# Performance work log

Measured on AMD Instinct MI355X. Metric: run time of the kernel, lower is better.

## Reference

```python
import jax, jax.numpy as jnp
import numpy as np

B, WS, DIM, HEADS, AGENT, PS = 128, 14, 256, 8, 49, 7
N = WS * WS


def conv(x, w, b, pad, groups=1):
    y = jax.lax.conv_general_dilated(x, w, (1, 1), [(pad, pad), (pad, pad)],
                                     dimension_numbers=('NCHW', 'OIHW', 'NCHW'),
                                     feature_group_count=groups)
    return y + b[None, :, None, None]


def bilinear_resize(x, oh, ow):
    # F.interpolate(mode='bilinear', align_corners=False) on last two dims
    ih, iw = x.shape[-2], x.shape[-1]
    def grid(ni, no):
        pos = np.maximum((np.arange(no) + 0.5) * (ni / no) - 0.5, 0.0)
        i0 = np.minimum(np.floor(pos).astype(np.int32), ni - 1)
        i1 = np.minimum(i0 + 1, ni - 1)
        return i0, i1, (pos - i0).astype(np.float32)
    i0h, i1h, lh = grid(ih, oh)
    i0w, i1w, lw = grid(iw, ow)
    xh = x[..., i0h, :] * (1.0 - lh)[:, None] + x[..., i1h, :] * lh[:, None]
    return xh[..., i0w] * (1.0 - lw) + xh[..., i1w] * lw


def rel_pos_index(h, w):
    coords = np.stack(np.meshgrid(np.arange(h), np.arange(w), indexing='ij')).reshape(2, -1)
    rel = (coords[:, :, None] - coords[:, None, :]).transpose(1, 2, 0).copy()
    rel[..., 0] += h - 1
    rel[..., 1] += w - 1
    rel[..., 0] *= 2 * w - 1
    return rel.sum(-1)  # (h*w, h*w)


def cbam(x, caa1_w, caa1_b, caa2_w, caa2_b, cam1_w, cam1_b, cam2_w, cam2_b, sa_w, sa_b):
    # ChannelAttention: both conv stacks act on 1x1 pooled maps -> only kernel centers matter
    avgp = x.mean((2, 3))
    t1 = jax.nn.relu(jnp.einsum('oi,bi->bo', caa1_w[:, :, 1, 1], avgp) + caa1_b)
    y1 = jax.nn.sigmoid(jnp.einsum('oi,bi->bo', caa2_w[:, :, 1, 1], t1) + caa2_b)
    mxp = x.max((2, 3))
    t2 = jax.nn.relu(jnp.einsum('oi,bi->bo', cam1_w[:, :, 0, 0], mxp) + cam1_b)
    y2 = jax.nn.sigmoid(jnp.einsum('oi,bi->bo', cam2_w[:, :, 0, 0], t2) + cam2_b)
    x = jax.nn.sigmoid(y1 + y2)[:, :, None, None] * x
    # Spatial attention
    mask = jnp.concatenate([x.mean(1, keepdims=True), x.max(1, keepdims=True)], axis=1)
    mask = jax.nn.sigmoid(conv(mask, sa_w, sa_b, 4))
    return x * mask


def chan_inter(x, ci1_w, ci1_b, bn_g, bn_b, ci2_w, ci2_b):
    # AdaptiveAvgPool2d(1) then 5x5 convs on 1x1 maps -> kernel-center matmuls; BN in eval mode
    p = x.mean((2, 3))
    t = jnp.einsum('oi,bi->bo', ci1_w[:, :, 2, 2], p) + ci1_b
    t = jax.nn.relu(bn_g * t * (1.0 / np.sqrt(1.0 + 1e-5)) + bn_b)
    return jnp.einsum('oi,bi->bo', ci2_w[:, :, 2, 2], t) + ci2_b


def setup_inputs() -> dict:
    key = jax.random.key(0)
    ks = jax.random.split(key, 40)
    d, r = DIM, DIM // 16
    p = lambda i, shape, s=0.02: jax.random.normal(ks[i], shape, jnp.float32) * s
    return {
        'x': jax.random.normal(ks[0], (B, N, d), jnp.float32),
        'h': WS,
        'w': WS,
        'lka_w': p(1, (3 * d, 1, 5, 5)), 'lka_b': p(2, (3 * d,)),
        'conv5_w': p(3, (d, d, 5, 5)), 'conv5_b': p(4, (d,)),
        'caa1_w': p(5, (r, d, 3, 3)), 'caa1_b': p(6, (r,)),
        'caa2_w': p(7, (d, r, 3, 3)), 'caa2_b': p(8, (d,)),
        'cam1_w': p(9, (r, d, 1, 1)), 'cam1_b': p(10, (r,)),
        'cam2_w': p(11, (d, r, 1, 1)), 'cam2_b': p(12, (d,)),
        'sa_w': p(13, (1, 2, 9, 9)), 'sa_b': p(14, (1,)),
        'ci1_w': p(15, (r, d, 5, 5)), 'ci1_b': p(16, (r,)),
        'bn_g': jnp.ones((r,), jnp.float32), 'bn_b': jnp.zeros((r,), jnp.float32),
        'ci2_w': p(17, (d, r, 5, 5)), 'ci2_b': p(18, (d,)),
        'rpb_table': p(19, ((2 * WS - 1) * (2 * WS - 1), HEADS)),
        'an_bias': p(20, (HEADS, AGENT, 7, 7)), 'na_bias': p(21, (HEADS, AGENT, 7, 7)),
        'ah_bias': p(22, (1, HEADS, AGENT, WS, 1)), 'aw_bias': p(23, (1, HEADS, AGENT, 1, WS)),
        'ha_bias': p(24, (1, HEADS, WS, 1, AGENT)), 'wa_bias': p(25, (1, HEADS, 1, WS, AGENT)),
        'dwc_w': p(26, (d, 1, 5, 5)), 'dwc_b': p(27, (d,)),
        'proj_w': p(28, (d, d)), 'proj_b': p(29, (d,)),
    }


def reference(x, h, w, lka_w, lka_b, conv5_w, conv5_b, caa1_w, caa1_b, caa2_w, caa2_b,
              cam1_w, cam1_b, cam2_w, cam2_b, sa_w, sa_b, ci1_w, ci1_b, bn_g, bn_b,
              ci2_w, ci2_b, rpb_table, an_bias, na_bias, ah_bias, aw_bias, ha_bias,
              wa_bias, dwc_w, dwc_b, proj_w, proj_b):
    b, n, c = x.shape
    heads, agent, ps = HEADS, AGENT, PS
    hd = c // heads
    scale = hd ** (-0.5)

    xc = jnp.transpose(x.reshape(b, h, w, c), (0, 3, 1, 2))  # (b,c,h,w)
    y = conv(xc, lka_w, lka_b, 2, groups=c)                   # depthwise, 3 outputs/group
    k_raw, v_raw, q_raw = y[:, :c], y[:, c:2 * c], y[:, 2 * c:]

    # v branch: conv5 then raw reshape-scramble (faithful to torch .reshape of NCHW), then CBAM
    v5 = jnp.transpose(conv(v_raw, conv5_w, conv5_b, 2).reshape(b, h, w, c), (0, 3, 1, 2))
    vc = cbam(v5, caa1_w, caa1_b, caa2_w, caa2_b, cam1_w, cam1_b, cam2_w, cam2_b, sa_w, sa_b)
    v_feat = jnp.transpose(vc.reshape(b, c, n), (0, 2, 1))    # (b,n,c)

    # adaptive avg/max pool 14->7 == exact 2x2 pooling
    at = q_raw.reshape(b, c, ps, h // ps, ps, w // ps).mean((3, 5)).reshape(b, c, agent).transpose(0, 2, 1)
    atk = k_raw.reshape(b, c, ps, h // ps, ps, w // ps).max((3, 5)).reshape(b, c, agent).transpose(0, 2, 1)

    # raw row-major reshapes of (b,c,h,w) into (b,n,heads,hd): faithful to torch
    q = q_raw.reshape(b, n, heads, hd).transpose(0, 2, 1, 3) * scale
    k = k_raw.reshape(b, n, heads, hd).transpose(0, 2, 1, 3)
    v = v_raw.reshape(b, n, heads, hd).transpose(0, 2, 1, 3)
    v1 = v_feat.reshape(b, n, heads, hd).transpose(0, 2, 1, 3)

    # full window attention with relative position bias
    idx = rel_pos_index(h, w)
    rpb = rpb_table[idx.reshape(-1)].reshape(n, n, heads).transpose(2, 0, 1)
    attn = jax.nn.softmax(jnp.einsum('bhid,bhjd->bhij', q, k) + rpb[None])
    x1 = jnp.einsum('bhij,bhjd->bhid', attn, v).transpose(0, 2, 1, 3).reshape(b, n, c)

    ar = x1.transpose(0, 2, 1).reshape(b, c, h, w)
    cmap = chan_inter(ar, ci1_w, ci1_b, bn_g, bn_b, ci2_w, ci2_b)  # (b,c)
    conv_x2 = jax.nn.sigmoid(cmap)[:, :, None, None] * jnp.transpose(q.reshape(b, h, w, c), (0, 3, 1, 2))

    # agent attention
    at_h = at.reshape(b, agent, heads, hd).transpose(0, 2, 1, 3)
    atk_h = atk.reshape(b, agent, heads, hd).transpose(0, 2, 1, 3)
    pb = bilinear_resize(an_bias, h, w).reshape(1, heads, agent, n) \
         + (ah_bias + aw_bias).reshape(1, heads, agent, n)
    agent_attn = jax.nn.softmax(jnp.einsum('bhad,bhnd->bhan', at_h * scale, k) + pb)
    agent_attn1 = jax.nn.softmax(jnp.einsum('bhad,bhnd->bhan', atk_h * scale, q) + pb)
    agent_v = jnp.einsum('bhan,bhnd->bhad', agent_attn, v1) + jnp.einsum('bhan,bhnd->bhad', agent_attn1, v)

    ab = bilinear_resize(na_bias, h, w).reshape(1, heads, agent, n).transpose(0, 1, 3, 2) \
         + (ha_bias + wa_bias).reshape(1, heads, n, agent)
    q_attn = jax.nn.softmax(jnp.einsum('bhnd,bhad->bhna', q * scale, at_h) + ab)
    k_attn = jax.nn.softmax(jnp.einsum('bhnd,bhad->bhna', k * scale, atk_h) + ab)
    xo = jnp.einsum('bhna,bhad->bhnd', q_attn + k_attn, agent_v).transpose(0, 2, 1, 3).reshape(b, n, c)

    xo = xo + jnp.transpose(conv(conv_x2, dwc_w, dwc_b, 2, groups=c), (0, 2, 3, 1)).reshape(b, n, c)
    qc = jnp.transpose(q.transpose(0, 2, 1, 3).reshape(b, h, w, c), (0, 3, 1, 2))
    xo = xo + jnp.transpose(conv(qc, dwc_w, dwc_b, 2, groups=c), (0, 2, 3, 1)).reshape(b, n, c)

    return xo @ proj_w.T + proj_b
```

## Files before the change

kernel.cpp:

```cpp
#include <hip/hip_runtime.h>

#define NB    128
#define NC    256
#define NPOS  196
#define NHEAD 8
#define NAG   49
#define YSTR  150528
#define VOFF  50176
#define QOFF  100352
#define SCL   0.17677669529663687f

#define WS_Y    0u
#define WS_V5   19267584u
#define WS_AT   25690112u
#define WS_ATK  27295744u
#define WS_CHG  28901376u
#define WS_CMAP 28934144u
#define WS_PBT  28966912u
#define WS_AB   29043744u
#define WS_X1S  29120576u
#define WS_AGV  29153344u
#define WS_XO   30758976u
#define WS_WT   37181504u
#define WS_CWT  37247040u

typedef __attribute__((ext_vector_type(8))) _Float16 half8;
typedef __attribute__((ext_vector_type(8))) short short8;
typedef __attribute__((ext_vector_type(4))) short short4v;
typedef __attribute__((ext_vector_type(4))) float f32x4;
typedef unsigned short ushort_t;
typedef unsigned int uint_t;

__device__ __forceinline__ float sigmoidf_(float x){ return 1.0f/(1.0f+__expf(-x)); }

__device__ __forceinline__ ushort_t f2h(float x){
  _Float16 h = (_Float16)x; return __builtin_bit_cast(ushort_t, h);
}
__device__ __forceinline__ float h2f(ushort_t u){
  return (float)__builtin_bit_cast(_Float16, u);
}

__device__ __forceinline__ float bilin7(const float* __restrict__ src, int i, int j){
  float pi = fmaxf(0.5f*(float)i - 0.25f, 0.f);
  int i0 = (int)pi; if (i0 > 6) i0 = 6;
  int i1 = i0 + 1;  if (i1 > 6) i1 = 6;
  float li = pi - (float)i0;
  float pj = fmaxf(0.5f*(float)j - 0.25f, 0.f);
  int j0 = (int)pj; if (j0 > 6) j0 = 6;
  int j1 = j0 + 1;  if (j1 > 6) j1 = 6;
  float lj = pj - (float)j0;
  float v00 = src[i0*7+j0], v01 = src[i0*7+j1];
  float v10 = src[i1*7+j0], v11 = src[i1*7+j1];
  float t0 = v00*(1.f-lj) + v01*lj;
  float t1 = v10*(1.f-lj) + v11*lj;
  return t0*(1.f-li) + t1*li;
}

__device__ __forceinline__ void conv5x5_row(const float* __restrict__ plane, int r,
                                            const float* __restrict__ w25, float* acc14){
  #pragma unroll
  for (int di = 0; di < 5; ++di){
    const float4* pr = (const float4*)(plane + (r+di)*20);
    float4 p0 = pr[0], p1 = pr[1], p2 = pr[2], p3 = pr[3], p4 = pr[4];
    float row[20] = {p0.x,p0.y,p0.z,p0.w, p1.x,p1.y,p1.z,p1.w, p2.x,p2.y,p2.z,p2.w,
                     p3.x,p3.y,p3.z,p3.w, p4.x,p4.y,p4.z,p4.w};
    #pragma unroll
    for (int dj = 0; dj < 5; ++dj){
      float w = w25[di*5+dj];
      #pragma unroll
      for (int j = 0; j < 14; ++j) acc14[j] = fmaf(row[j+dj], w, acc14[j]);
    }
  }
}

__global__ void k_pb(const float* __restrict__ an, const float* __restrict__ ah,
                     const float* __restrict__ aw, float* __restrict__ PBT){
  int t = blockIdx.x*256 + threadIdx.x;
  if (t >= NHEAD*NPOS*NAG) return;
  int a = t % NAG;
  int r = t / NAG;
  int n = r % NPOS;
  int h = r / NPOS;
  int i = n/14, j = n - (n/14)*14;
  float v = bilin7(an + ((size_t)h*NAG + a)*49, i, j);
  v += ah[((size_t)h*NAG + a)*14 + i] + aw[((size_t)h*NAG + a)*14 + j];
  PBT[t] = v;
}

__global__ void k_ab(const float* __restrict__ na, const float* __restrict__ ha,
                     const float* __restrict__ wa, float* __restrict__ AB){
  int t = blockIdx.x*256 + threadIdx.x;
  if (t >= NHEAD*NPOS*NAG) return;
  int a = t % NAG;
  int r = t / NAG;
  int n = r % NPOS;
  int h = r / NPOS;
  int i = n/14, j = n - (n/14)*14;
  float v = bilin7(na + ((size_t)h*NAG + a)*49, i, j);
  v += ha[((size_t)h*14 + i)*NAG + a] + wa[((size_t)h*14 + j)*NAG + a];
  AB[t] = v;
}

__global__ void k_wt(const float* __restrict__ pw, float* __restrict__ WT){
  int t = blockIdx.x*256 + threadIdx.x;
  if (t >= 65536) return;
  int k = t >> 8, c = t & 255;
  WT[t] = pw[c*256 + k];
}

__global__ void k_cw2(const float* __restrict__ cw, ushort_t* __restrict__ Wh){
  int t = blockIdx.x*256 + threadIdx.x;
  if (t >= 1638400) return;
  int ci = t & 255;
  int r  = t >> 8;
  int co = r & 255;
  int tap = r >> 8;
  Wh[t] = f2h(cw[((size_t)co*256 + ci)*25 + tap]);
}

__global__ __launch_bounds__(256) void k_lka(const float* __restrict__ x, const float* __restrict__ lw,
                                             const float* __restrict__ lb, float* __restrict__ Y){
  int b = blockIdx.x >> 3, gb = blockIdx.x & 7;
  int g0 = gb*32;
  __shared__ __align__(16) float pl[32*360];
  int tid = threadIdx.x;
  for (int t = tid; t < 32*360; t += 256) pl[t] = 0.f;
  __syncthreads();
  for (int t = tid; t < 32*196; t += 256){
    int gl = t & 31, s = t >> 5;
    int i = s/14, j = s - i*14;
    pl[gl*360 + (i+2)*20 + j + 2] = x[((size_t)b*196 + s)*256 + g0 + gl];
  }
  __syncthreads();
  for (int t = tid; t < 96*14; t += 256){
    int ocl = t/14, r = t - ocl*14;
    int o  = g0*3 + ocl;
    int gl = ocl/3;
    float w25[25];
    #pragma unroll
    for (int u = 0; u < 25; ++u) w25[u] = lw[o*25 + u];
    float acc[14];
    float bv = lb[o];
    #pragma unroll
    for (int j = 0; j < 14; ++j) acc[j] = bv;
    conv5x5_row(&pl[gl*360], r, w25, acc);
    float* dst = Y + ((size_t)b*768 + o)*196 + r*14;
    #pragma unroll
    for (int j = 0; j < 14; ++j) dst[j] = acc[j];
  }
}

__global__ __launch_bounds__(256, 2) void k_conv5(const float* __restrict__ Y,
    const ushort_t* __restrict__ Wh, const float* __restrict__ cb, float* __restrict__ V5){
  int b = blockIdx.x >> 2, cog = blockIdx.x & 3;
  int co0 = cog*64;
  __shared__ __align__(16) ushort_t Pt[360*40];
  __shared__ __align__(16) ushort_t Wsm[5*64*40];
  __shared__ float T[32*200];
  int tid  = threadIdx.x;
  int lane = tid & 63, wv = tid >> 6;
  int mrow = lane & 15, quad = lane >> 4;

  for (int t = tid; t < 7200; t += 256) ((uint_t*)Pt)[t] = 0;

  int prow[4];
  #pragma unroll
  for (int mt = 0; mt < 4; ++mt){
    int s = wv*64 + mt*16 + mrow;
    int p0 = 0;
    if (s < 196){ int i = s/14, j = s - i*14; p0 = i*20 + j; }
    prow[mt] = p0;
  }

  f32x4 acc[4][4];
  #pragma unroll
  for (int mt = 0; mt < 4; ++mt)
    #pragma unroll
    for (int nt = 0; nt < 4; ++nt) acc[mt][nt] = (f32x4){0.f,0.f,0.f,0.f};

  const float* src = Y + (size_t)b*YSTR + VOFF;
  int wco = tid >> 2, wpart = tid & 3;

  #pragma unroll 1
  for (int cc = 0; cc < 8; ++cc){
    __syncthreads();
    if (tid < 196){
      int s = tid; int i = s/14, j = s - i*14;
      int p = (i+2)*20 + (j+2);
      const float* s0 = src + (cc*32)*196 + s;
      #pragma unroll
      for (int cp = 0; cp < 16; ++cp){
        float v0 = s0[(2*cp)*196];
        float v1 = s0[(2*cp+1)*196];
        uint_t pk = (uint_t)f2h(v0) | ((uint_t)f2h(v1) << 16);
        int q = cp >> 2;
        *(uint_t*)&Pt[p*40 + (((q ^ p) & 3) << 3) + ((2*cp) & 7)] = pk;
      }
    }
    #pragma unroll 1
    for (int di = 0; di < 5; ++di){
      __syncthreads();
      #pragma unroll
      for (int tp = 0; tp < 5; ++tp){
        int tap = di*5 + tp;
        const short8 g = *(const short8*)(Wh + ((size_t)tap*256 + co0 + wco)*256 + cc*32 + wpart*8);
        *(short8*)&Wsm[(tp*64 + wco)*40 + (((wpart ^ wco) & 3) << 3)] = g;
      }
      __syncthreads();
      #pragma unroll
      for (int dj = 0; dj < 5; ++dj){
        half8 a[4], bb[4];
        #pragma unroll
        for (int nt = 0; nt < 4; ++nt){
          int co = nt*16 + mrow;
          bb[nt] = *(const half8*)&Wsm[(dj*64 + co)*40 + (((quad ^ co) & 3) << 3)];
        }
        #pragma unroll
        for (int mt = 0; mt < 4; ++mt){
          int p = prow[mt] + di*20 + dj;
          a[mt] = *(const half8*)&Pt[p*40 + (((quad ^ p) & 3) << 3)];
        }
        #pragma unroll
        for (int mt = 0; mt < 4; ++mt)
          #pragma unroll
          for (int nt = 0; nt < 4; ++nt)
            acc[mt][nt] = __builtin_amdgcn_mfma_f32_16x16x32_f16(a[mt], bb[nt], acc[mt][nt], 0, 0, 0);
      }
    }
  }

  #pragma unroll
  for (int hf = 0; hf < 2; ++hf){
    __syncthreads();
    #pragma unroll
    for (int ntl = 0; ntl < 2; ++ntl){
      int nt = hf*2 + ntl;
      int col = ntl*16 + mrow;
      #pragma unroll
      for (int mt = 0; mt < 4; ++mt){
        int sbase = wv*64 + mt*16 + quad*4;
        #pragma unroll
        for (int r = 0; r < 4; ++r){
          int s = sbase + r;
          if (s < 196) T[col*200 + s] = acc[mt][nt][r];
        }
      }
    }
    __syncthreads();
    for (int t = tid; t < 6272; t += 256){
      int cl = t / 196;
      int f = (co0 + hf*32)*196 + t;
      float val = T[t + cl*4] + cb[co0 + hf*32 + cl];
      V5[(size_t)b*50176 + (size_t)(f & 255)*196 + (f >> 8)] = val;
    }
  }
}

__global__ __launch_bounds__(256) void k_pool(const float* __restrict__ Y, float* __restrict__ AT, float* __restrict__ ATK){
  int b = blockIdx.x; int c = threadIdx.x;
  const float* qp = Y + ((size_t)b*768 + 512 + c)*196;
  const float* kp = Y + ((size_t)b*768 + c)*196;
  for (int a = 0; a < 49; ++a){
    int p1 = a/7, p2 = a - p1*7;
    int s = p1*28 + p2*2;
    float q0 = qp[s], q1 = qp[s+1], q2 = qp[s+14], q3 = qp[s+15];
    AT[((size_t)b*49 + a)*256 + c] = 0.25f*(q0+q1+q2+q3);
    float k0 = kp[s], k1 = kp[s+1], k2 = kp[s+14], k3 = kp[s+15];
    ATK[((size_t)b*49 + a)*256 + c] = fmaxf(fmaxf(k0,k1), fmaxf(k2,k3));
  }
}

__global__ __launch_bounds__(256) void k_cbam_a(const float* __restrict__ V5,
    const float* __restrict__ caa1w, const float* __restrict__ caa1b,
    const float* __restrict__ caa2w, const float* __restrict__ caa2b,
    const float* __restrict__ cam1w, const float* __restrict__ cam1b,
    const float* __restrict__ cam2w, const float* __restrict__ cam2b,
    float* __restrict__ CHG){
  int b = blockIdx.x, c = threadIdx.x;
  __shared__ float avg[256], mx[256], t1[16], t2[16];
  const float* pp = V5 + ((size_t)b*256 + c)*196;
  float s = 0.f, m = -1e30f;
  for (int i = 0; i < 196; ++i){ float v = pp[i]; s += v; m = fmaxf(m, v); }
  avg[c] = s * (1.0f/196.0f); mx[c] = m;
  __syncthreads();
  if (c < 16){
    float a1 = caa1b[c], a2 = cam1b[c];
    #pragma unroll 4
    for (int k = 0; k < 256; ++k){
      a1 = fmaf(caa1w[(c*256 + k)*9 + 4], avg[k], a1);
      a2 = fmaf(cam1w[c*256 + k], mx[k], a2);
    }
    t1[c] = fmaxf(a1, 0.f);
    t2[c] = fmaxf(a2, 0.f);
  }
  __syncthreads();
  float y1 = caa2b[c], y2 = cam2b[c];
  #pragma unroll
  for (int k = 0; k < 16; ++k){
    y1 = fmaf(caa2w[(c*16 + k)*9 + 4], t1[k], y1);
    y2 = fmaf(cam2w[c*16 + k], t2[k], y2);
  }
  CHG[b*256 + c] = sigmoidf_(sigmoidf_(y1) + sigmoidf_(y2));
}

__global__ __launch_bounds__(256) void k_cbam_b(float* __restrict__ V5, const float* __restrict__ CHG,
    const float* __restrict__ saw, const float* __restrict__ sab){
  int b = blockIdx.x; int tid = threadIdx.x;
  __shared__ float chg[256];
  __shared__ float mp[22*22], xp[22*22];
  __shared__ float mk[196];
  chg[tid] = CHG[b*256 + tid];
  for (int t = tid; t < 484; t += 256){ mp[t] = 0.f; xp[t] = 0.f; }
  __syncthreads();
  if (tid < 196){
    int i = tid/14, j = tid - i*14;
    float s = 0.f, m = -1e30f;
    const float* vb = V5 + (size_t)b*256*196 + tid;
    for (int c = 0; c < 256; ++c){
      float v = chg[c] * vb[c*196];
      s += v; m = fmaxf(m, v);
    }
    mp[(i+4)*22 + j+4] = s*(1.f/256.f);
    xp[(i+4)*22 + j+4] = m;
  }
  __syncthreads();
  if (tid < 196){
    int i = tid/14, j = tid - i*14;
    float acc = sab[0];
    for (int di = 0; di < 9; ++di){
      #pragma unroll
      for (int dj = 0; dj < 9; ++dj){
        acc = fmaf(mp[(i+di)*22 + j+dj], saw[di*9+dj], acc);
        acc = fmaf(xp[(i+di)*22 + j+dj], saw[81 + di*9+dj], acc);
      }
    }
    mk[tid] = sigmoidf_(acc);
  }
  __syncthreads();
  if (tid < 196){
    float m = mk[tid];
    float* vb = V5 + (size_t)b*256*196 + tid;
    for (int c = 0; c < 256; ++c) vb[c*196] = chg[c]*vb[c*196]*m;
  }
}

__global__ __launch_bounds__(256) void k_attn(const float* __restrict__ Y, const float* __restrict__ rpbt,
                                              float* __restrict__ X1S){
  int b = blockIdx.x >> 3, h = blockIdx.x & 7;
  __shared__ float rp[729];
  __shared__ float xs[196*33];
  int tid = threadIdx.x;
  for (int t = tid; t < 729; t += 256) rp[t] = rpbt[t*8 + h];
  __syncthreads();
  const float* yb = Y + (size_t)b*YSTR;
  if (tid < 196){
    int n = tid;
    float q[32];
    {
      const float4* q4 = (const float4*)(yb + QOFF + (size_t)n*256 + h*32);
      #pragma unroll
      for (int u = 0; u < 8; ++u){
        float4 v = q4[u];
        q[4*u] = v.x*SCL; q[4*u+1] = v.y*SCL; q[4*u+2] = v.z*SCL; q[4*u+3] = v.w*SCL;
      }
    }
    int ri = n/14, ci = n - ri*14;
    int bidx = (ri + 13)*27 + (ci + 13);
    float acc[32];
    #pragma unroll
    for (int d = 0; d < 32; ++d) acc[d] = 0.f;
    float l = 0.f;
    int rj = 0, cj = 0;
    for (int j = 0; j < 196; ++j){
      const float4* k4 = (const float4*)(yb + (size_t)j*256 + h*32);
      float s0 = 0.f, s1 = 0.f;
      #pragma unroll
      for (int u = 0; u < 8; u += 2){
        float4 a = k4[u], bb = k4[u+1];
        s0 = fmaf(q[4*u+0],a.x, fmaf(q[4*u+1],a.y, fmaf(q[4*u+2],a.z, fmaf(q[4*u+3],a.w, s0))));
        s1 = fmaf(q[4*u+4],bb.x, fmaf(q[4*u+5],bb.y, fmaf(q[4*u+6],bb.z, fmaf(q[4*u+7],bb.w, s1))));
      }
      float s = s0 + s1 + rp[bidx - rj*27 - cj];
      float p = __expf(s);
      l += p;
      const float4* v4 = (const float4*)(yb + VOFF + (size_t)j*256 + h*32);
      #pragma unroll
      for (int u = 0; u < 8; ++u){
        float4 vv = v4[u];
        acc[4*u]   = fmaf(p, vv.x, acc[4*u]);
        acc[4*u+1] = fmaf(p, vv.y, acc[4*u+1]);
        acc[4*u+2] = fmaf(p, vv.z, acc[4*u+2]);
        acc[4*u+3] = fmaf(p, vv.w, acc[4*u+3]);
      }
      if (++cj == 14){ cj = 0; ++rj; }
    }
    float inv = 1.f/l;
    #pragma unroll
    for (int d = 0; d < 32; ++d) xs[n*33 + d] = acc[d]*inv;
  }
  __syncthreads();
  if (tid < 32){
    float s = 0.f;
    for (int n = 0; n < 196; ++n) s += xs[n*33 + tid];
    X1S[(size_t)b*256 + h*32 + tid] = s*(1.f/196.f);
  }
}

__global__ __launch_bounds__(256) void k_cinter(const float* __restrict__ X1S,
    const float* __restrict__ ci1w, const float* __restrict__ ci1b,
    const float* __restrict__ bng, const float* __restrict__ bnb,
    const float* __restrict__ ci2w, const float* __restrict__ ci2b, float* __restrict__ CMAP){
  int b = blockIdx.x, c = threadIdx.x;
  __shared__ float p[256], tt[16];
  p[c] = X1S[b*256 + c];
  __syncthreads();
  if (c < 16){
    float a = ci1b[c];
    #pragma unroll 4
    for (int k = 0; k < 256; ++k) a = fmaf(ci1w[(c*256+k)*25 + 12], p[k], a);
    const float invs = 0.9999950000375f;
    tt[c] = fmaxf(fmaf(bng[c]*invs, a, bnb[c]), 0.f);
  }
  __syncthreads();
  float a = ci2b[c];
  #pragma unroll
  for (int k = 0; k < 16; ++k) a = fmaf(ci2w[(c*16+k)*25 + 12], tt[k], a);
  CMAP[b*256 + c] = sigmoidf_(a);
}

__global__ __launch_bounds__(256) void k_agentv(const float* __restrict__ Y, const float* __restrict__ V5,
    const float* __restrict__ AT, const float* __restrict__ ATK,
    const float* __restrict__ PBT, float* __restrict__ AGV){
  int b = blockIdx.x >> 3, h = blockIdx.x & 7;
  __shared__ __align__(16) ushort_t ST[64*232];
  __shared__ __align__(16) ushort_t R[8704];
  __shared__ float psum[4*64];
  __shared__ float inv0s[64], inv1s[64];
  int tid = threadIdx.x, wv = tid >> 6, lane = tid & 63;
  int mrow = lane & 15, quad = lane >> 4;
  const float* yb = Y + (size_t)b*YSTR;
  ushort_t* Kh = R;
  ushort_t* Ah = R + 6656;
  ushort_t* Vt = R;
  f32x4 out0[2], out1[2];

  for (int t = tid; t < 512; t += 256){
    int a = t >> 3, c2 = 208 + ((t & 7) << 1);
    *(uint_t*)&ST[a*232 + c2] = 0;
  }

  #pragma unroll 1
  for (int pass = 0; pass < 2; ++pass){
    for (int t = tid; t < 192; t += 256) ((uint_t*)Kh)[3136 + t] = 0;
    for (int t = tid; t < 240; t += 256) ((uint_t*)Ah)[784 + t] = 0;
    {
      const float* rsrc = yb + (pass ? QOFF : 0) + h*32;
      for (int t = tid; t < 3136; t += 256){
        int n = t >> 4, dp = (t & 15) << 1;
        const float2 v = *(const float2*)(rsrc + (size_t)n*256 + dp);
        ((uint_t*)Kh)[n*16 + (dp >> 1)] = (uint_t)f2h(v.x) | ((uint_t)f2h(v.y) << 16);
      }
      const float* asrc = (pass ? ATK : AT) + (size_t)b*49*256 + h*32;
      for (int t = tid; t < 784; t += 256){
        int a = t >> 4, dp = (t & 15) << 1;
        const float2 v = *(const float2*)(asrc + (size_t)a*256 + dp);
        ((uint_t*)Ah)[a*16 + (dp >> 1)] = (uint_t)f2h(v.x) | ((uint_t)f2h(v.y) << 16);
      }
    }
    __syncthreads();
    {
      float lscl = pass ? 0.03125f : SCL;
      int ag = wv*16 + mrow;
      half8 bfr = *(const half8*)&Ah[ag*32 + quad*8];
      #pragma unroll 1
      for (int mt = 0; mt < 13; ++mt){
        half8 afr = *(const half8*)&Kh[(mt*16 + mrow)*32 + quad*8];
        f32x4 c = (f32x4){0.f,0.f,0.f,0.f};
        c = __builtin_amdgcn_mfma_f32_16x16x32_f16(afr, bfr, c, 0, 0, 0);
        int n0 = mt*16 + quad*4;
        short4v pk;
        #pragma unroll
        for (int r = 0; r < 4; ++r){
          int n = n0 + r;
          float pb = PBT[((size_t)h*196 + n)*49 + ag];
          float e = (n < 196) ? __expf(fmaf(c[r], lscl, pb)) : 0.f;
          pk[r] = (short)f2h(e);
        }
        *(short4v*)&ST[ag*232 + n0] = pk;
      }
    }
    __syncthreads();
    {
      int a = tid >> 2, q = tid & 3;
      float s = 0.f;
      #pragma unroll
      for (int u = 0; u < 7; ++u){
        short8 v8 = *(const short8*)&ST[a*232 + q*56 + u*8];
        #pragma unroll
        for (int e = 0; e < 8; ++e) s += h2f((ushort_t)v8[e]);
      }
      psum[q*64 + a] = s;
    }
    if (pass == 0){
      const float* vsrc = V5 + (size_t)b*50176 + h*32*196;
      for (int t = tid; t < 3136; t += 256){
        int d = t / 98, np = t - (t/98)*98;
        const float2 v = *(const float2*)(vsrc + (size_t)d*196 + 2*np);
        *(uint_t*)&Vt[d*232 + 2*np] = (uint_t)f2h(v.x) | ((uint_t)f2h(v.y) << 16);
      }
    } else {
      const float* vsrc = yb + VOFF + h*32;
      for (int t = tid; t < 3136; t += 256){
        int d = t / 98, np = t - (t/98)*98;
        float v0 = vsrc[(size_t)(2*np)*256 + d];
        float v1 = vsrc[(size_t)(2*np+1)*256 + d];
        *(uint_t*)&Vt[d*232 + 2*np] = (uint_t)f2h(v0) | ((uint_t)f2h(v1) << 16);
      }
    }
    for (int t = tid; t < 448; t += 256){
      int d = t / 14, c2 = 196 + 2*(t - (t/14)*14);
      *(uint_t*)&Vt[d*232 + c2] = 0;
    }
    __syncthreads();
    {
      f32x4* outp = pass ? out1 : out0;
      #pragma unroll
      for (int nt = 0; nt < 2; ++nt){
        f32x4 c = (f32x4){0.f,0.f,0.f,0.f};
        #pragma unroll
        for (int ks = 0; ks < 7; ++ks){
          half8 afr = *(const half8*)&ST[(wv*16 + mrow)*232 + ks*32 + quad*8];
          half8 bfr = *(const half8*)&Vt[(nt*16 + mrow)*232 + ks*32 + quad*8];
          c = __builtin_amdgcn_mfma_f32_16x16x32_f16(afr, bfr, c, 0, 0, 0);
        }
        outp[nt] = c;
      }
      if (tid < 64){
        float s = psum[tid] + psum[64+tid] + psum[128+tid] + psum[192+tid];
        float* invp = pass ? inv1s : inv0s;
        invp[tid] = 1.f / s;
      }
    }
    __syncthreads();
  }
  #pragma unroll
  for (int nt = 0; nt < 2; ++nt){
    int d = nt*16 + mrow;
    #pragma unroll
    for (int r = 0; r < 4; ++r){
      int a = wv*16 + quad*4 + r;
      if (a < 49)
        AGV[(((size_t)(b*8 + h)*49) + a)*32 + d] = out0[nt][r]*inv0s[a] + out1[nt][r]*inv1s[a];
    }
  }
}

__global__ __launch_bounds__(256) void k_xo1(const float* __restrict__ Y,
    const float* __restrict__ AT, const float* __restrict__ ATK,
    const float* __restrict__ AB, const float* __restrict__ AGV, float* __restrict__ XO){
  int b = blockIdx.x >> 3, h = blockIdx.x & 7;
  __shared__ __align__(16) ushort_t ST[208*72];
  __shared__ __align__(16) ushort_t Kh[208*32];
  __shared__ __align__(16) ushort_t Ah[64*32];
  __shared__ __align__(16) ushort_t AGVt[32*64];
  __shared__ float invs[208];
  int tid = threadIdx.x, wv = tid >> 6, lane = tid & 63;
  int mrow = lane & 15, quad = lane >> 4;
  const float* yb = Y + (size_t)b*YSTR;
  f32x4 acc[4][2];
  #pragma unroll
  for (int i = 0; i < 4; ++i){
    acc[i][0] = (f32x4){0.f,0.f,0.f,0.f};
    acc[i][1] = (f32x4){0.f,0.f,0.f,0.f};
  }

  for (int t = tid; t < 1664; t += 256){
    int rw = t >> 3, c2 = 48 + ((t & 7) << 1);
    *(uint_t*)&ST[rw*72 + c2] = 0;
  }
  {
    const float* agvb = AGV + (size_t)(b*8 + h)*49*32;
    for (int t = tid; t < 2048; t += 256){
      int d = t >> 6, a = t & 63;
      AGVt[d*64 + a] = (a < 49) ? f2h(agvb[a*32 + d]) : (ushort_t)0;
    }
  }

  #pragma unroll 1
  for (int pass = 0; pass < 2; ++pass){
    {
      const float* rsrc = yb + (pass ? 0 : QOFF) + h*32;
      for (int t = tid; t < 3136; t += 256){
        int n = t >> 4, dp = (t & 15) << 1;
        const float2 v = *(const float2*)(rsrc + (size_t)n*256 + dp);
        ((uint_t*)Kh)[n*16 + (dp >> 1)] = (uint_t)f2h(v.x) | ((uint_t)f2h(v.y) << 16);
      }
      const float* asrc = (pass ? ATK : AT) + (size_t)b*49*256 + h*32;
      for (int t = tid; t < 784; t += 256){
        int a = t >> 4, dp = (t & 15) << 1;
        const float2 v = *(const float2*)(asrc + (size_t)a*256 + dp);
        ((uint_t*)Ah)[a*16 + (dp >> 1)] = (uint_t)f2h(v.x) | ((uint_t)f2h(v.y) << 16);
      }
    }
    __syncthreads();
    {
      float lscl = pass ? SCL : 0.03125f;
      int ag = wv*16 + mrow;
      half8 bfr = *(const half8*)&Ah[ag*32 + quad*8];
      #pragma unroll 1
      for (int mt = 0; mt < 13; ++mt){
        half8 afr = *(const half8*)&Kh[(mt*16 + mrow)*32 + quad*8];
        f32x4 c = (f32x4){0.f,0.f,0.f,0.f};
        c = __builtin_amdgcn_mfma_f32_16x16x32_f16(afr, bfr, c, 0, 0, 0);
        #pragma unroll
        for (int r = 0; r < 4; ++r){
          int n = mt*16 + quad*4 + r;
          if (n < 196 && ag < 49){
            float e = __expf(fmaf(c[r], lscl, AB[((size_t)h*196 + n)*49 + ag]));
            ST[n*72 + ag] = f2h(e);
          }
        }
      }
    }
    __syncthreads();
    if (tid < 196){
      float s = 0.f;
      #pragma unroll
      for (int u = 0; u < 7; ++u){
        short8 v8 = *(const short8*)&ST[tid*72 + u*8];
        #pragma unroll
        for (int e = 0; e < 8; ++e) s += h2f((ushort_t)v8[e]);
      }
      invs[tid] = 1.f / s;
    }
    __syncthreads();
    {
      int i = 0;
      #pragma unroll 1
      for (int mt = wv; mt < 13; mt += 4, ++i){
        #pragma unroll
        for (int nt = 0; nt < 2; ++nt){
          f32x4 c = (f32x4){0.f,0.f,0.f,0.f};
          #pragma unroll
          for (int ks = 0; ks < 2; ++ks){
            half8 afr = *(const half8*)&ST[(mt*16 + mrow)*72 + ks*32 + quad*8];
            half8 bfr = *(const half8*)&AGVt[(nt*16 + mrow)*64 + ks*32 + quad*8];
            c = __builtin_amdgcn_mfma_f32_16x16x32_f16(afr, bfr, c, 0, 0, 0);
          }
          #pragma unroll
          for (int r = 0; r < 4; ++r){
            int n = mt*16 + quad*4 + r;
            if (n < 196) acc[i][nt][r] = fmaf(c[r], invs[n], acc[i][nt][r]);
          }
        }
      }
    }
    __syncthreads();
  }
  {
    int i = 0;
    #pragma unroll 1
    for (int mt = wv; mt < 13; mt += 4, ++i){
      #pragma unroll
      for (int nt = 0; nt < 2; ++nt){
        #pragma unroll
        for (int r = 0; r < 4; ++r){
          int n = mt*16 + quad*4 + r;
          if (n < 196)
            XO[((size_t)b*196 + n)*256 + h*32 + nt*16 + mrow] = acc[i][nt][r];
        }
      }
    }
  }
}

__global__ __launch_bounds__(256) void k_dwc(const float* __restrict__ Y, const float* __restrict__ CMAP,
    const float* __restrict__ dw, const float* __restrict__ db, float* __restrict__ XO){
  int b = blockIdx.x >> 3, cg = blockIdx.x & 7;
  int c0 = cg*32;
  __shared__ __align__(16) float pl[32*360];
  int tid = threadIdx.x;
  for (int t = tid; t < 32*360; t += 256) pl[t] = 0.f;
  __syncthreads();
  const float* yq = Y + (size_t)b*YSTR + QOFF;
  for (int t = tid; t < 32*196; t += 256){
    int cl = t & 31, s = t >> 5;
    int c = c0 + cl;
    int G = s*256 + c;
    int hh = G / 6272;
    int rem = G - hh*6272;
    int n = rem >> 5, d = rem & 31;
    float cx2 = CMAP[b*256 + c] * yq[n*256 + hh*32 + d];
    float qc  = yq[G];
    float v = SCL*(cx2 + qc);
    int i = s/14, j = s - i*14;
    pl[cl*360 + (i+2)*20 + j + 2] = v;
  }
  __syncthreads();
  for (int t = tid; t < 32*14; t += 256){
    int cl = t/14, r = t - cl*14;
    int c = c0 + cl;
    float w25[25];
    #pragma unroll
    for (int u = 0; u < 25; ++u) w25[u] = dw[c*25 + u];
    float acc[14];
    float b2 = 2.f*db[c];
    #pragma unroll
    for (int j = 0; j < 14; ++j) acc[j] = b2;
    conv5x5_row(&pl[cl*360], r, w25, acc);
    float* dst = XO + ((size_t)b*196 + r*14)*256 + c;
    #pragma unroll
    for (int j = 0; j < 14; ++j) dst[j*256] += acc[j];
  }
}

__global__ __launch_bounds__(256) void k_proj(const float* __restrict__ XO, const float* __restrict__ WT,
    const float* __restrict__ pbias, float* __restrict__ OUT){
  int bb = blockIdx.x / 7, nt = blockIdx.x % 7;
  int n0 = nt*28;
  int c = threadIdx.x;
  const float* xb = XO + ((size_t)bb*196 + n0)*256;
  float acc[28];
  #pragma unroll
  for (int r = 0; r < 28; ++r) acc[r] = 0.f;
  for (int k = 0; k < 256; k += 4){
    float w0 = WT[(k+0)*256 + c];
    float w1 = WT[(k+1)*256 + c];
    float w2 = WT[(k+2)*256 + c];
    float w3 = WT[(k+3)*256 + c];
    #pragma unroll
    for (int r = 0; r < 28; ++r){
      float4 xv = *(const float4*)(xb + r*256 + k);
      acc[r] = fmaf(xv.x, w0, fmaf(xv.y, w1, fmaf(xv.z, w2, fmaf(xv.w, w3, acc[r]))));
    }
  }
  float bv = pbias[c];
  float* dst = OUT + ((size_t)bb*196 + n0)*256 + c;
  #pragma unroll
  for (int r = 0; r < 28; ++r) dst[r*256] = acc[r] + bv;
}

extern "C" void kernel_launch(void* const* d_in, const int* in_sizes, int n_in,
                              void* d_out, int out_size, void* d_ws, size_t ws_size,
                              hipStream_t stream){
  (void)in_sizes; (void)n_in; (void)out_size; (void)ws_size;
  const float* x       = (const float*)d_in[0];
  const float* lka_w   = (const float*)d_in[3];
  const float* lka_b   = (const float*)d_in[4];
  const float* conv5_w = (const float*)d_in[5];
  const float* conv5_b = (const float*)d_in[6];
  const float* caa1_w  = (const float*)d_in[7];
  const float* caa1_b  = (const float*)d_in[8];
  const float* caa2_w  = (const float*)d_in[9];
  const float* caa2_b  = (const float*)d_in[10];
  const float* cam1_w  = (const float*)d_in[11];
  const float* cam1_b  = (const float*)d_in[12];
  const float* cam2_w  = (const float*)d_in[13];
  const float* cam2_b  = (const float*)d_in[14];
  const float* sa_w    = (const float*)d_in[15];
  const float* sa_b    = (const float*)d_in[16];
  const float* ci1_w   = (const float*)d_in[17];
  const float* ci1_b   = (const float*)d_in[18];
  const float* bn_g    = (const float*)d_in[19];
  const float* bn_b    = (const float*)d_in[20];
  const float* ci2_w   = (const float*)d_in[21];
  const float* ci2_b   = (const float*)d_in[22];
  const float* rpbt    = (const float*)d_in[23];
  const float* an_bias = (const float*)d_in[24];
  const float* na_bias = (const float*)d_in[25];
  const float* ah_bias = (const float*)d_in[26];
  const float* aw_bias = (const float*)d_in[27];
  const float* ha_bias = (const float*)d_in[28];
  const float* wa_bias = (const float*)d_in[29];
  const float* dwc_w   = (const float*)d_in[30];
  const float* dwc_b   = (const float*)d_in[31];
  const float* proj_w  = (const float*)d_in[32];
  const float* proj_b  = (const float*)d_in[33];
  float* out = (float*)d_out;
  float* ws = (float*)d_ws;

  float* Y    = ws + WS_Y;
  float* V5   = ws + WS_V5;
  float* AT   = ws + WS_AT;
  float* ATK  = ws + WS_ATK;
  float* CHG  = ws + WS_CHG;
  float* CMAP = ws + WS_CMAP;
  float* PBT  = ws + WS_PBT;
  float* AB   = ws + WS_AB;
  float* X1S  = ws + WS_X1S;
  float* AGV  = ws + WS_AGV;
  float* XO   = ws + WS_XO;
  float* WT   = ws + WS_WT;
  ushort_t* Wh = (ushort_t*)(ws + WS_CWT);

  k_pb   <<<301, 256, 0, stream>>>(an_bias, ah_bias, aw_bias, PBT);
  k_ab   <<<301, 256, 0, stream>>>(na_bias, ha_bias, wa_bias, AB);
  k_wt   <<<256, 256, 0, stream>>>(proj_w, WT);
  k_cw2  <<<6400, 256, 0, stream>>>(conv5_w, Wh);
  k_lka  <<<1024, 256, 0, stream>>>(x, lka_w, lka_b, Y);
  k_conv5<<<512, 256, 0, stream>>>(Y, Wh, conv5_b, V5);
  k_pool <<<128, 256, 0, stream>>>(Y, AT, ATK);
  k_cbam_a<<<128, 256, 0, stream>>>(V5, caa1_w, caa1_b, caa2_w, caa2_b,
                                    cam1_w, cam1_b, cam2_w, cam2_b, CHG);
  k_cbam_b<<<128, 256, 0, stream>>>(V5, CHG, sa_w, sa_b);
  k_attn <<<1024, 256, 0, stream>>>(Y, rpbt, X1S);
  k_cinter<<<128, 256, 0, stream>>>(X1S, ci1_w, ci1_b, bn_g, bn_b, ci2_w, ci2_b, CMAP);
  k_agentv<<<1024, 256, 0, stream>>>(Y, V5, AT, ATK, PBT, AGV);
  k_xo1  <<<1024, 256, 0, stream>>>(Y, AT, ATK, AB, AGV, XO);
  k_dwc  <<<1024, 256, 0, stream>>>(Y, CMAP, dwc_w, dwc_b, XO);
  k_proj <<<896, 256, 0, stream>>>(XO, WT, proj_b, out);
}
```

Baseline: 893.6 us.

## Pre-pack conv5 weights for direct global fragment loads and swizzle attention LDS tiles

```diff
diff --git a/kernel.cpp b/kernel.cpp
--- a/kernel.cpp
+++ b/kernel.cpp
@@ -111,10 +111,13 @@
 __global__ void k_cw2(const float* __restrict__ cw, ushort_t* __restrict__ Wh){
   int t = blockIdx.x*256 + threadIdx.x;
   if (t >= 1638400) return;
-  int ci = t & 255;
-  int r  = t >> 8;
-  int co = r & 255;
-  int tap = r >> 8;
+  int e   = t & 7;
+  int r   = t >> 3;
+  int tap = r % 25;
+  int r2  = r / 25;
+  int co  = r2 & 255;
+  int ccq = r2 >> 8;
+  int ci  = (ccq >> 2)*32 + (ccq & 3)*8 + e;
   Wh[t] = f2h(cw[((size_t)co*256 + ci)*25 + tap]);
 }
 
@@ -155,7 +158,6 @@
   int b = blockIdx.x >> 2, cog = blockIdx.x & 3;
   int co0 = cog*64;
   __shared__ __align__(16) ushort_t Pt[360*40];
-  __shared__ __align__(16) ushort_t Wsm[5*64*40];
   __shared__ float T[32*200];
   int tid  = threadIdx.x;
   int lane = tid & 63, wv = tid >> 6;
@@ -179,53 +181,41 @@
     for (int nt = 0; nt < 4; ++nt) acc[mt][nt] = (f32x4){0.f,0.f,0.f,0.f};
 
   const float* src = Y + (size_t)b*YSTR + VOFF;
-  int wco = tid >> 2, wpart = tid & 3;
 
   #pragma unroll 1
   for (int cc = 0; cc < 8; ++cc){
     __syncthreads();
-    if (tid < 196){
-      int s = tid; int i = s/14, j = s - i*14;
-      int p = (i+2)*20 + (j+2);
-      const float* s0 = src + (cc*32)*196 + s;
-      #pragma unroll
-      for (int cp = 0; cp < 16; ++cp){
-        float v0 = s0[(2*cp)*196];
-        float v1 = s0[(2*cp+1)*196];
-        uint_t pk = (uint_t)f2h(v0) | ((uint_t)f2h(v1) << 16);
-        int q = cp >> 2;
-        *(uint_t*)&Pt[p*40 + (((q ^ p) & 3) << 3) + ((2*cp) & 7)] = pk;
-      }
-    }
-    #pragma unroll 1
-    for (int di = 0; di < 5; ++di){
-      __syncthreads();
-      #pragma unroll
-      for (int tp = 0; tp < 5; ++tp){
-        int tap = di*5 + tp;
-        const short8 g = *(const short8*)(Wh + ((size_t)tap*256 + co0 + wco)*256 + cc*32 + wpart*8);
-        *(short8*)&Wsm[(tp*64 + wco)*40 + (((wpart ^ wco) & 3) << 3)] = g;
-      }
-      __syncthreads();
-      #pragma unroll
-      for (int dj = 0; dj < 5; ++dj){
-        half8 a[4], bb[4];
+    for (int t = tid; t < 3136; t += 256){
+      int cp = t / 196, s = t - cp*196;
+      int i = s/14, j = s - i*14;
+      const float* s0 = src + (size_t)(cc*32 + 2*cp)*196 + s;
+      float v0 = s0[0];
+      float v1 = s0[196];
+      ((uint_t*)Pt)[((i+2)*20 + j + 2)*20 + cp] =
+          (uint_t)f2h(v0) | ((uint_t)f2h(v1) << 16);
+    }
+    __syncthreads();
+
+    const ushort_t* wb[4];
+    #pragma unroll
+    for (int nt = 0; nt < 4; ++nt)
+      wb[nt] = Wh + ((size_t)(cc*4 + quad)*256 + co0 + nt*16 + mrow)*200;
+
+    #pragma unroll
+    for (int tap = 0; tap < 25; ++tap){
+      int di = tap / 5, dj = tap - (tap/5)*5;
+      half8 a[4], bb[4];
+      #pragma unroll
+      for (int nt = 0; nt < 4; ++nt)
+        bb[nt] = *(const half8*)(wb[nt] + tap*8);
+      #pragma unroll
+      for (int mt = 0; mt < 4; ++mt)
+        a[mt] = *(const half8*)&Pt[(prow[mt] + di*20 + dj)*40 + quad*8];
+      #pragma unroll
+      for (int mt = 0; mt < 4; ++mt)
         #pragma unroll
-        for (int nt = 0; nt < 4; ++nt){
-          int co = nt*16 + mrow;
-          bb[nt] = *(const half8*)&Wsm[(dj*64 + co)*40 + (((quad ^ co) & 3) << 3)];
-        }
-        #pragma unroll
-        for (int mt = 0; mt < 4; ++mt){
-          int p = prow[mt] + di*20 + dj;
-          a[mt] = *(const half8*)&Pt[p*40 + (((quad ^ p) & 3) << 3)];
-        }
-        #pragma unroll
-        for (int mt = 0; mt < 4; ++mt)
-          #pragma unroll
-          for (int nt = 0; nt < 4; ++nt)
-            acc[mt][nt] = __builtin_amdgcn_mfma_f32_16x16x32_f16(a[mt], bb[nt], acc[mt][nt], 0, 0, 0);
-      }
+        for (int nt = 0; nt < 4; ++nt)
+          acc[mt][nt] = __builtin_amdgcn_mfma_f32_16x16x32_f16(a[mt], bb[nt], acc[mt][nt], 0, 0, 0);
     }
   }
 
@@ -438,6 +428,7 @@
   __shared__ float inv0s[64], inv1s[64];
   int tid = threadIdx.x, wv = tid >> 6, lane = tid & 63;
   int mrow = lane & 15, quad = lane >> 4;
+  int sw8 = ((quad ^ ((mrow >> 1) & 3)) << 3);
   const float* yb = Y + (size_t)b*YSTR;
   ushort_t* Kh = R;
   ushort_t* Ah = R + 6656;
@@ -456,25 +447,27 @@
     {
       const float* rsrc = yb + (pass ? QOFF : 0) + h*32;
       for (int t = tid; t < 3136; t += 256){
-        int n = t >> 4, dp = (t & 15) << 1;
-        const float2 v = *(const float2*)(rsrc + (size_t)n*256 + dp);
-        ((uint_t*)Kh)[n*16 + (dp >> 1)] = (uint_t)f2h(v.x) | ((uint_t)f2h(v.y) << 16);
+        int n = t >> 4, w = t & 15;
+        const float2 v = *(const float2*)(rsrc + (size_t)n*256 + (w << 1));
+        int ws = (((w >> 2) ^ ((n >> 1) & 3)) << 2) | (w & 3);
+        ((uint_t*)Kh)[n*16 + ws] = (uint_t)f2h(v.x) | ((uint_t)f2h(v.y) << 16);
       }
       const float* asrc = (pass ? ATK : AT) + (size_t)b*49*256 + h*32;
       for (int t = tid; t < 784; t += 256){
-        int a = t >> 4, dp = (t & 15) << 1;
-        const float2 v = *(const float2*)(asrc + (size_t)a*256 + dp);
-        ((uint_t*)Ah)[a*16 + (dp >> 1)] = (uint_t)f2h(v.x) | ((uint_t)f2h(v.y) << 16);
+        int a = t >> 4, w = t & 15;
+        const float2 v = *(const float2*)(asrc + (size_t)a*256 + (w << 1));
+        int ws = (((w >> 2) ^ ((a >> 1) & 3)) << 2) | (w & 3);
+        ((uint_t*)Ah)[a*16 + ws] = (uint_t)f2h(v.x) | ((uint_t)f2h(v.y) << 16);
       }
     }
     __syncthreads();
     {
       float lscl = pass ? 0.03125f : SCL;
       int ag = wv*16 + mrow;
-      half8 bfr = *(const half8*)&Ah[ag*32 + quad*8];
+      half8 bfr = *(const half8*)&Ah[ag*32 + sw8];
       #pragma unroll 1
       for (int mt = 0; mt < 13; ++mt){
-        half8 afr = *(const half8*)&Kh[(mt*16 + mrow)*32 + quad*8];
+        half8 afr = *(const half8*)&Kh[(mt*16 + mrow)*32 + sw8];
         f32x4 c = (f32x4){0.f,0.f,0.f,0.f};
         c = __builtin_amdgcn_mfma_f32_16x16x32_f16(afr, bfr, c, 0, 0, 0);
         int n0 = mt*16 + quad*4;
@@ -566,6 +559,7 @@
   __shared__ float invs[208];
   int tid = threadIdx.x, wv = tid >> 6, lane = tid & 63;
   int mrow = lane & 15, quad = lane >> 4;
+  int sw8 = ((quad ^ ((mrow >> 1) & 3)) << 3);
   const float* yb = Y + (size_t)b*YSTR;
   f32x4 acc[4][2];
   #pragma unroll
@@ -582,7 +576,8 @@
     const float* agvb = AGV + (size_t)(b*8 + h)*49*32;
     for (int t = tid; t < 2048; t += 256){
       int d = t >> 6, a = t & 63;
-      AGVt[d*64 + a] = (a < 49) ? f2h(agvb[a*32 + d]) : (ushort_t)0;
+      int as = ((((a >> 3) ^ (d & 7)) & 7) << 3) | (a & 7);
+      AGVt[d*64 + as] = (a < 49) ? f2h(agvb[a*32 + d]) : (ushort_t)0;
     }
   }
 
@@ -591,25 +586,27 @@
     {
       const float* rsrc = yb + (pass ? 0 : QOFF) + h*32;
       for (int t = tid; t < 3136; t += 256){
-        int n = t >> 4, dp = (t & 15) << 1;
-        const float2 v = *(const float2*)(rsrc + (size_t)n*256 + dp);
-        ((uint_t*)Kh)[n*16 + (dp >> 1)] = (uint_t)f2h(v.x) | ((uint_t)f2h(v.y) << 16);
+        int n = t >> 4, w = t & 15;
+        const float2 v = *(const float2*)(rsrc + (size_t)n*256 + (w << 1));
+        int ws = (((w >> 2) ^ ((n >> 1) & 3)) << 2) | (w & 3);
+        ((uint_t*)Kh)[n*16 + ws] = (uint_t)f2h(v.x) | ((uint_t)f2h(v.y) << 16);
       }
       const float* asrc = (pass ? ATK : AT) + (size_t)b*49*256 + h*32;
       for (int t = tid; t < 784; t += 256){
-        int a = t >> 4, dp = (t & 15) << 1;
-        const float2 v = *(const float2*)(asrc + (size_t)a*256 + dp);
-        ((uint_t*)Ah)[a*16 + (dp >> 1)] = (uint_t)f2h(v.x) | ((uint_t)f2h(v.y) << 16);
+        int a = t >> 4, w = t & 15;
+        const float2 v = *(const float2*)(asrc + (size_t)a*256 + (w << 1));
+        int ws = (((w >> 2) ^ ((a >> 1) & 3)) << 2) | (w & 3);
+        ((uint_t*)Ah)[a*16 + ws] = (uint_t)f2h(v.x) | ((uint_t)f2h(v.y) << 16);
       }
     }
     __syncthreads();
     {
       float lscl = pass ? SCL : 0.03125f;
       int ag = wv*16 + mrow;
-      half8 bfr = *(const half8*)&Ah[ag*32 + quad*8];
+      half8 bfr = *(const half8*)&Ah[ag*32 + sw8];
       #pragma unroll 1
       for (int mt = 0; mt < 13; ++mt){
-        half8 afr = *(const half8*)&Kh[(mt*16 + mrow)*32 + quad*8];
+        half8 afr = *(const half8*)&Kh[(mt*16 + mrow)*32 + sw8];
         f32x4 c = (f32x4){0.f,0.f,0.f,0.f};
         c = __builtin_amdgcn_mfma_f32_16x16x32_f16(afr, bfr, c, 0, 0, 0);
         #pragma unroll
@@ -644,7 +641,7 @@
           #pragma unroll
           for (int ks = 0; ks < 2; ++ks){
             half8 afr = *(const half8*)&ST[(mt*16 + mrow)*72 + ks*32 + quad*8];
-            half8 bfr = *(const half8*)&AGVt[(nt*16 + mrow)*64 + ks*32 + quad*8];
+            half8 bfr = *(const half8*)&AGVt[(nt*16 + mrow)*64 + ((((ks*4 + quad) ^ (mrow & 7)) & 7) << 3)];
             c = __builtin_amdgcn_mfma_f32_16x16x32_f16(afr, bfr, c, 0, 0, 0);
           }
           #pragma unroll
```

New measurement: 933.0 us. 4.4% more time.
